# Kernel optimization log

Hardware: AMD Instinct MI355X
Metric: run time of the kernel (lower is better)

The kernel has to match this reference:

```python
import jax, jax.numpy as jnp
import numpy as np

B, S, D, H = 4, 1024, 1024, 16
DK = D // H


def _linear_params(key, scale):
    kw, kb = jax.random.split(key)
    W = jax.random.normal(kw, (D, D), dtype=jnp.float32) * scale
    b = jax.random.normal(kb, (D,), dtype=jnp.float32) * 0.01
    return W, b


def setup_inputs() -> dict:
    key = jax.random.key(0)
    ks = jax.random.split(key, 12)
    scale = 1.0 / np.sqrt(D)
    inp = {
        "query": jax.random.normal(ks[0], (B, S, D), dtype=jnp.float32),
        "key": jax.random.normal(ks[1], (B, S, D), dtype=jnp.float32),
        "value": jax.random.normal(ks[2], (B, S, D), dtype=jnp.float32),
        "time_k": jax.random.normal(ks[3], (B, S, D), dtype=jnp.float32),
        "time_v": jax.random.normal(ks[4], (B, S, D), dtype=jnp.float32),
        "mask": jnp.zeros((B, 1, S, S), dtype=jnp.float32),
    }
    names = ["Wq", "bq", "Wk", "bk", "Wv", "bv", "Wtk", "btk", "Wtv", "btv", "Wm", "bm"]
    for i in range(6):
        W, b = _linear_params(ks[5 + i], scale)
        inp[names[2 * i]] = W
        inp[names[2 * i + 1]] = b
    return inp


def _split_heads(x):
    # [B,S,D] -> [B,H,S,DK]
    b, s, _ = x.shape
    return x.reshape(b, s, H, DK).transpose(0, 2, 1, 3)


def reference(query, key, value, time_k, time_v, mask,
              Wq, bq, Wk, bk, Wv, bv, Wtk, btk, Wtv, btv, Wm, bm):
    q = _split_heads(query @ Wq + bq)
    k = _split_heads(key @ Wk + bk)
    v = _split_heads(value @ Wv + bv)
    t_k = _split_heads(time_k @ Wtk + btk)
    t_v = _split_heads(time_v @ Wtv + btv)

    # scores[b,h,i,j] = q_i . k_j + t_k_i . q_j  (note second term uses q on the key axis)
    scores = jnp.einsum("bhid,bhjd->bhij", q, k) + jnp.einsum("bhid,bhjd->bhij", t_k, q)
    # module divides by sqrt(d_model) (query.size(-1)), not sqrt(d_k)
    scores = scores / jnp.sqrt(jnp.float32(D)) + mask
    probs = jax.nn.softmax(scores, axis=-1)

    # dropout is identity (p=0 / eval); squeeze(-2) is a no-op for S>1
    context = jnp.einsum("bhij,bhjd->bhid", probs, v) + jnp.einsum("bhij,bhjd->bhid", probs, t_v)
    x = context.transpose(0, 2, 1, 3).reshape(query.shape[0], -1, D)
    return x @ Wm + bm
```

## Files before the change

kernel.cpp:

```cpp
#include <hip/hip_runtime.h>
#include <hip/hip_bf16.h>
#include <cstdint>
#include <cstddef>

typedef __bf16 bf16;
typedef bf16 bf16x8 __attribute__((ext_vector_type(8)));
typedef bf16 bf16x4 __attribute__((ext_vector_type(4)));
typedef float f32x4 __attribute__((ext_vector_type(4)));
typedef unsigned int u32;

#define DEV static __device__ __forceinline__

DEV f32x4 mfma16(bf16x8 a, bf16x8 b, f32x4 c) {
    return __builtin_amdgcn_mfma_f32_16x16x32_bf16(a, b, c, 0, 0, 0);
}

DEV f32x4 shflx4(f32x4 v, int m) {
    f32x4 r;
    for (int i = 0; i < 4; ++i) r[i] = __shfl_xor(v[i], m, 64);
    return r;
}

DEV bf16x8 cvt8(const float* p) {
    float4 f0 = *(const float4*)p;
    float4 f1 = *(const float4*)(p + 4);
    bf16x8 v;
    v[0] = (bf16)f0.x; v[1] = (bf16)f0.y; v[2] = (bf16)f0.z; v[3] = (bf16)f0.w;
    v[4] = (bf16)f1.x; v[5] = (bf16)f1.y; v[6] = (bf16)f1.z; v[7] = (bf16)f1.w;
    return v;
}

DEV void glo(const bf16* g, bf16* l) {
    __builtin_amdgcn_global_load_lds(
        (const __attribute__((address_space(1))) u32*)g,
        (__attribute__((address_space(3))) u32*)l,
        16, 0, 0);
}

struct PrepArgs {
    const float* w[6];
    const float* act[6];
    bf16* wt;
    bf16* actbf[6];
};

__global__ __launch_bounds__(256) void prep_kernel(PrepArgs p)
{
    const int z = blockIdx.z;
    const int t = threadIdx.x;
    if (z < 6) {
        __shared__ bf16 tile[64][72];
        const float* src = p.w[z];
        bf16* out = p.wt + (size_t)z * 1024 * 1024;
        const int r = t >> 3, c8 = (t & 7) * 8;
        const int row0 = blockIdx.y * 64, col0 = blockIdx.x * 64;
        *(bf16x8*)&tile[r][c8]      = cvt8(&src[(size_t)(row0 + r) * 1024 + col0 + c8]);
        *(bf16x8*)&tile[r + 32][c8] = cvt8(&src[(size_t)(row0 + r + 32) * 1024 + col0 + c8]);
        __syncthreads();
        for (int half = 0; half < 2; ++half) {
            int rr = r + half * 32;
            bf16x8 v;
            for (int j = 0; j < 8; ++j) v[j] = tile[c8 + j][rr];
            *(bf16x8*)&out[(size_t)(col0 + rr) * 1024 + row0 + c8] = v;
        }
    } else {
        const float* src = p.act[z - 6];
        bf16* dst = p.actbf[z - 6];
        const size_t chunk = (size_t)(blockIdx.y * 16 + blockIdx.x) * 16384;
        for (int c = 0; c < 8; ++c) {
            const size_t off = chunk + (size_t)c * 2048 + (size_t)t * 8;
            *(bf16x8*)&dst[off] = cvt8(&src[off]);
        }
    }
}

__global__ __launch_bounds__(256) void vsum_kernel(bf16* __restrict__ a,
                                                   const bf16* __restrict__ b)
{
    const size_t off = ((size_t)blockIdx.x * 256 + threadIdx.x) * 16;
    for (int c = 0; c < 2; ++c) {
        bf16x8 x = *(const bf16x8*)&a[off + c * 8];
        bf16x8 y = *(const bf16x8*)&b[off + c * 8];
        bf16x8 s;
        for (int e = 0; e < 8; ++e) s[e] = (bf16)((float)x[e] + (float)y[e]);
        *(bf16x8*)&a[off + c * 8] = s;
    }
}

struct ProjArgs {
    const void* A[5];
    const void* A2[5];
    const bf16* W[5];
    const bf16* W2[5];
    const float* bias[5];
    const float* bias2[5];
    bf16* out[5];
    int vst[5];
};

template<bool AF32>
__global__ __launch_bounds__(256) void proj_gemm(ProjArgs pa)
{
    const int z = blockIdx.z;
    const void* A   = pa.A[z];
    const void* A2p = pa.A2[z];
    const bf16* W   = pa.W[z];
    const bf16* W2  = pa.W2[z];
    const int m0 = blockIdx.y * 128, n0 = blockIdx.x * 128;
    __shared__ bf16 As[128 * 64];
    __shared__ bf16 Bs[128 * 64];
    const int t = threadIdx.x, lane = t & 63, w = t >> 6;
    const int ln = lane & 15, qd = lane >> 4;
    const int wm0 = (w >> 1) * 64, wn0 = (w & 1) * 64;
    const int srow = t >> 1, shalf = (t & 1) * 32;
    const int sub0 = w * 4;
    const int r8 = lane >> 3, c8 = (lane & 7) * 8;
    f32x4 acc[4][4];
    for (int i = 0; i < 4; ++i)
        for (int j = 0; j < 4; ++j)
            acc[i][j] = (f32x4){0.f, 0.f, 0.f, 0.f};
    const int npair = A2p ? 2 : 1;
    for (int pair = 0; pair < npair; ++pair) {
        const void* Ap = pair ? A2p : A;
        const bf16* Wp = pair ? W2 : W;
        for (int ks = 0; ks < 16; ++ks) {
            const int bk = ks * 64;
            __syncthreads();
            for (int i = 0; i < 4; ++i) {
                const int row = (sub0 + i) * 8 + r8;
                glo(&Wp[(size_t)(n0 + row) * 1024 + bk + c8], &Bs[(sub0 + i) * 512]);
            }
            if (AF32) {
                const float* src = &((const float*)Ap)[(size_t)(m0 + srow) * 1024 + bk + shalf];
                bf16* dst = &As[srow * 64 + shalf];
                *(bf16x8*)(dst)      = cvt8(src);
                *(bf16x8*)(dst + 8)  = cvt8(src + 8);
                *(bf16x8*)(dst + 16) = cvt8(src + 16);
                *(bf16x8*)(dst + 24) = cvt8(src + 24);
            } else {
                const bf16* Ab = (const bf16*)Ap;
                for (int i = 0; i < 4; ++i) {
                    const int row = (sub0 + i) * 8 + r8;
                    glo(&Ab[(size_t)(m0 + row) * 1024 + bk + c8], &As[(sub0 + i) * 512]);
                }
            }
            __syncthreads();
            for (int kc = 0; kc < 2; ++kc) {
                bf16x8 af[4], bfr[4];
                for (int mi = 0; mi < 4; ++mi)
                    af[mi] = *(const bf16x8*)&As[(wm0 + mi * 16 + ln) * 64 + kc * 32 + qd * 8];
                for (int ni = 0; ni < 4; ++ni)
                    bfr[ni] = *(const bf16x8*)&Bs[(wn0 + ni * 16 + ln) * 64 + kc * 32 + qd * 8];
                for (int mi = 0; mi < 4; ++mi)
                    for (int ni = 0; ni < 4; ++ni)
                        acc[mi][ni] = mfma16(af[mi], bfr[ni], acc[mi][ni]);
            }
        }
    }
    const float* bias  = pa.bias[z];
    const float* bias2 = pa.bias2[z];
    bf16* out = pa.out[z];
    const int vst = pa.vst[z];
    for (int ni = 0; ni < 4; ++ni) {
        const int n = n0 + wn0 + ni * 16 + ln;
        const float bv = bias[n] + (bias2 ? bias2[n] : 0.0f);
        for (int mi = 0; mi < 4; ++mi) {
            const int mbase = m0 + wm0 + mi * 16 + qd * 4;
            f32x4 v = acc[mi][ni];
            if (vst) {
                const int b = mbase >> 10, s = mbase & 1023;
                bf16x4 pk;
                for (int r = 0; r < 4; ++r) pk[r] = (bf16)(v[r] + bv);
                *(bf16x4*)&out[((size_t)(b * 1024 + n)) * 1024 + s] = pk;
            } else {
                for (int r = 0; r < 4; ++r)
                    out[(size_t)(mbase + r) * 1024 + n] = (bf16)(v[r] + bv);
            }
        }
    }
}

__global__ __launch_bounds__(256) void attn4_kernel(
    const bf16* __restrict__ Qb, const bf16* __restrict__ Kb, const bf16* __restrict__ TKb,
    const bf16* __restrict__ VsT, const bf16* __restrict__ maskbf,
    bf16* __restrict__ ctx)
{
    const int h = blockIdx.x, it = blockIdx.y, b = blockIdx.z;
    const int i0 = it * 128;
    __shared__ bf16 Ks[64 * 64];
    __shared__ bf16 QJs[64 * 64];
    __shared__ bf16 Vs[64 * 64];
    __shared__ bf16 Ms[128 * 64];
    __shared__ bf16 Ps[128][72];
    const int t = threadIdx.x, lane = t & 63, w = t >> 6;
    const int ln = lane & 15, qd = lane >> 4;
    const size_t baseQ = ((size_t)b * 1024) * 1024 + (size_t)h * 64;
    const size_t MMc = (size_t)1024 * 1024;

    bf16x8 qf[2][2], tkf[2][2];
    for (int si = 0; si < 2; ++si) {
        const size_t row = (size_t)(i0 + w * 32 + si * 16 + ln);
        for (int kc = 0; kc < 2; ++kc) {
            qf[si][kc]  = *(const bf16x8*)&Qb [baseQ + row * 1024 + kc * 32 + qd * 8];
            tkf[si][kc] = *(const bf16x8*)&TKb[baseQ + row * 1024 + kc * 32 + qd * 8];
        }
    }

    f32x4 O[2][4];
    f32x4 psum[2];
    for (int si = 0; si < 2; ++si) {
        psum[si] = (f32x4){0.f, 0.f, 0.f, 0.f};
        for (int dc = 0; dc < 4; ++dc) O[si][dc] = (f32x4){0.f, 0.f, 0.f, 0.f};
    }

    const float c1 = 0.045084439f;
    const float c2 = 1.442695041f;

    for (int jt = 0; jt < 16; ++jt) {
        const int j0 = jt * 64;
        __syncthreads();
        {
            const int rr = lane >> 3, cb = (lane & 7) * 8;
            for (int i = 0; i < 10; ++i) {
                const int u = w * 10 + i;
                if (u < 8) {
                    glo(&Kb[baseQ + (size_t)(j0 + u * 8 + rr) * 1024 + cb], &Ks[u * 512]);
                } else if (u < 16) {
                    const int s = u - 8;
                    glo(&Qb[baseQ + (size_t)(j0 + s * 8 + rr) * 1024 + cb], &QJs[s * 512]);
                } else if (u < 24) {
                    const int s = u - 16;
                    glo(&VsT[((size_t)b * 1024 + h * 64 + s * 8 + rr) * 1024 + j0 + cb],
                        &Vs[s * 512]);
                } else {
                    const int s = u - 24;
                    glo(&maskbf[(size_t)b * MMc + (size_t)(i0 + s * 8 + rr) * 1024 + j0 + cb],
                        &Ms[s * 512]);
                }
            }
        }
        __syncthreads();

        f32x4 sc[2][4];
        for (int jc = 0; jc < 4; ++jc) {
            bf16x8 kf[2], qjf[2];
            for (int kc = 0; kc < 2; ++kc) {
                kf[kc]  = *(const bf16x8*)&Ks [(jc * 16 + ln) * 64 + kc * 32 + qd * 8];
                qjf[kc] = *(const bf16x8*)&QJs[(jc * 16 + ln) * 64 + kc * 32 + qd * 8];
            }
            for (int si = 0; si < 2; ++si) {
                f32x4 a = (f32x4){0.f, 0.f, 0.f, 0.f};
                a = mfma16(qf[si][0], kf[0], a);
                a = mfma16(qf[si][1], kf[1], a);
                a = mfma16(tkf[si][0], qjf[0], a);
                a = mfma16(tkf[si][1], qjf[1], a);
                sc[si][jc] = a;
            }
        }
        for (int si = 0; si < 2; ++si) {
            const int ibl = w * 32 + si * 16 + qd * 4;
            for (int jc = 0; jc < 4; ++jc) {
                const int jl = jc * 16 + ln;
                for (int r = 0; r < 4; ++r) {
                    const float mv = (float)Ms[(ibl + r) * 64 + jl];
                    const float p = exp2f(fmaf(sc[si][jc][r], c1, mv * c2));
                    psum[si][r] += p;
                    Ps[ibl + r][jl] = (bf16)p;
                }
            }
        }
        for (int kc = 0; kc < 2; ++kc) {
            bf16x8 pa[2], vb[4];
            for (int si = 0; si < 2; ++si)
                pa[si] = *(const bf16x8*)&Ps[w * 32 + si * 16 + ln][kc * 32 + qd * 8];
            for (int dc = 0; dc < 4; ++dc)
                vb[dc] = *(const bf16x8*)&Vs[(dc * 16 + ln) * 64 + kc * 32 + qd * 8];
            for (int si = 0; si < 2; ++si)
                for (int dc = 0; dc < 4; ++dc)
                    O[si][dc] = mfma16(pa[si], vb[dc], O[si][dc]);
        }
    }

    for (int si = 0; si < 2; ++si) {
        for (int m = 1; m <= 8; m <<= 1) psum[si] += shflx4(psum[si], m);
        f32x4 rl;
        for (int r = 0; r < 4; ++r) rl[r] = 1.0f / psum[si][r];
        const int ibase = i0 + w * 32 + si * 16 + qd * 4;
        for (int dc = 0; dc < 4; ++dc) {
            const int d = h * 64 + dc * 16 + ln;
            f32x4 v = O[si][dc] * rl;
            for (int r = 0; r < 4; ++r)
                ctx[((size_t)b * 1024 + ibase + r) * 1024 + d] = (bf16)v[r];
        }
    }
}

__global__ __launch_bounds__(256) void out_gemm(
    const bf16* __restrict__ A, const bf16* __restrict__ W,
    const float* __restrict__ bias, float* __restrict__ out)
{
    const int n0 = blockIdx.x * 128, m0 = blockIdx.y * 64;
    __shared__ bf16 As[64 * 64];
    __shared__ bf16 Bs[128 * 64];
    const int t = threadIdx.x, lane = t & 63, w = t >> 6;
    const int ln = lane & 15, qd = lane >> 4;
    const int wn0 = w * 32;
    const int rr = lane >> 3, cb = (lane & 7) * 8;
    f32x4 acc[4][2];
    for (int i = 0; i < 4; ++i)
        for (int j = 0; j < 2; ++j)
            acc[i][j] = (f32x4){0.f, 0.f, 0.f, 0.f};
    for (int ks = 0; ks < 16; ++ks) {
        const int bk = ks * 64;
        __syncthreads();
        for (int i = 0; i < 6; ++i) {
            const int u = w * 6 + i;
            if (u < 8) {
                const int r8 = u * 8 + rr;
                glo(&A[(size_t)(m0 + r8) * 1024 + bk + cb], &As[u * 512]);
            } else {
                const int sub = u - 8, r8 = sub * 8 + rr;
                glo(&W[(size_t)(n0 + r8) * 1024 + bk + cb], &Bs[sub * 512]);
            }
        }
        __syncthreads();
        for (int kc = 0; kc < 2; ++kc) {
            bf16x8 af[4], bfr[2];
            for (int mi = 0; mi < 4; ++mi)
                af[mi] = *(const bf16x8*)&As[(mi * 16 + ln) * 64 + kc * 32 + qd * 8];
            for (int ni = 0; ni < 2; ++ni)
                bfr[ni] = *(const bf16x8*)&Bs[(wn0 + ni * 16 + ln) * 64 + kc * 32 + qd * 8];
            for (int mi = 0; mi < 4; ++mi)
                for (int ni = 0; ni < 2; ++ni)
                    acc[mi][ni] = mfma16(af[mi], bfr[ni], acc[mi][ni]);
        }
    }
    for (int ni = 0; ni < 2; ++ni) {
        const int n = n0 + wn0 + ni * 16 + ln;
        const float bv = bias[n];
        for (int mi = 0; mi < 4; ++mi) {
            const int mbase = m0 + mi * 16 + qd * 4;
            f32x4 v = acc[mi][ni];
            for (int r = 0; r < 4; ++r)
                out[(size_t)(mbase + r) * 1024 + n] = v[r] + bv;
        }
    }
}

extern "C" void kernel_launch(void* const* d_in, const int* in_sizes, int n_in,
                              void* d_out, int out_size, void* d_ws, size_t ws_size,
                              hipStream_t stream)
{
    (void)in_sizes; (void)n_in; (void)out_size;
    const float* query  = (const float*)d_in[0];
    const float* key    = (const float*)d_in[1];
    const float* value  = (const float*)d_in[2];
    const float* time_k = (const float*)d_in[3];
    const float* time_v = (const float*)d_in[4];
    const float* mask   = (const float*)d_in[5];
    const float* Wq  = (const float*)d_in[6];  const float* bq  = (const float*)d_in[7];
    const float* Wk  = (const float*)d_in[8];  const float* bk  = (const float*)d_in[9];
    const float* Wv  = (const float*)d_in[10]; const float* bv  = (const float*)d_in[11];
    const float* Wtk = (const float*)d_in[12]; const float* btk = (const float*)d_in[13];
    const float* Wtv = (const float*)d_in[14]; const float* btv = (const float*)d_in[15];
    const float* Wm  = (const float*)d_in[16]; const float* bm  = (const float*)d_in[17];

    bf16* ws = (bf16*)d_ws;
    const size_t MM = (size_t)1024 * 1024;
    bf16* WT = ws;
    bf16* maskbf = (bf16*)d_out;

    PrepArgs pp;
    pp.w[0] = Wq; pp.w[1] = Wk; pp.w[2] = Wv; pp.w[3] = Wtk; pp.w[4] = Wtv; pp.w[5] = Wm;
    pp.wt = WT;

    const bool big = ws_size >= (size_t)(46 * MM * sizeof(bf16));

    if (big) {
        bf16* qbf  = ws + 6 * MM;
        bf16* kbf  = ws + 10 * MM;
        bf16* vbf  = ws + 14 * MM;
        bf16* tkbf = ws + 18 * MM;
        bf16* tvbf = ws + 22 * MM;
        bf16* Qb   = ws + 26 * MM;
        bf16* Kb   = ws + 30 * MM;
        bf16* TKb  = ws + 34 * MM;
        bf16* VsTa = ws + 38 * MM;
        bf16* VsTb = ws + 42 * MM;
        bf16* ctx  = ws + 6 * MM;
        pp.act[0] = query; pp.act[1] = key; pp.act[2] = value;
        pp.act[3] = time_k; pp.act[4] = time_v; pp.act[5] = mask;
        pp.actbf[0] = qbf; pp.actbf[1] = kbf; pp.actbf[2] = vbf;
        pp.actbf[3] = tkbf; pp.actbf[4] = tvbf; pp.actbf[5] = maskbf;
        prep_kernel<<<dim3(16, 16, 12), 256, 0, stream>>>(pp);

        ProjArgs pa;
        for (int i = 0; i < 5; ++i) { pa.A2[i] = nullptr; pa.W2[i] = nullptr; pa.bias2[i] = nullptr; }
        pa.A[0] = qbf;  pa.W[0] = WT + 0 * MM; pa.bias[0] = bq;  pa.out[0] = Qb;   pa.vst[0] = 0;
        pa.A[1] = kbf;  pa.W[1] = WT + 1 * MM; pa.bias[1] = bk;  pa.out[1] = Kb;   pa.vst[1] = 0;
        pa.A[2] = tkbf; pa.W[2] = WT + 3 * MM; pa.bias[2] = btk; pa.out[2] = TKb;  pa.vst[2] = 0;
        pa.A[3] = vbf;  pa.W[3] = WT + 2 * MM; pa.bias[3] = bv;  pa.out[3] = VsTa; pa.vst[3] = 1;
        pa.A[4] = tvbf; pa.W[4] = WT + 4 * MM; pa.bias[4] = btv; pa.out[4] = VsTb; pa.vst[4] = 1;
        proj_gemm<false><<<dim3(8, 32, 5), 256, 0, stream>>>(pa);

        vsum_kernel<<<dim3(1024), 256, 0, stream>>>(VsTa, VsTb);
        attn4_kernel<<<dim3(16, 8, 4), 256, 0, stream>>>(
            Qb, Kb, TKb, VsTa, maskbf, ctx);
        out_gemm<<<dim3(8, 64), 256, 0, stream>>>(ctx, WT + 5 * MM, bm, (float*)d_out);
    } else {
        bf16* Qb  = ws + 6 * MM;
        bf16* Kb  = ws + 10 * MM;
        bf16* TKb = ws + 14 * MM;
        bf16* VsT = ws + 18 * MM;
        bf16* ctx = ws + 22 * MM;
        pp.act[0] = mask;
        for (int i = 1; i < 6; ++i) pp.act[i] = nullptr;
        pp.actbf[0] = maskbf;
        for (int i = 1; i < 6; ++i) pp.actbf[i] = nullptr;
        prep_kernel<<<dim3(16, 16, 7), 256, 0, stream>>>(pp);

        ProjArgs pa;
        for (int i = 0; i < 5; ++i) { pa.A2[i] = nullptr; pa.W2[i] = nullptr; pa.bias2[i] = nullptr; }
        pa.A[0] = value;  pa.A2[0] = time_v; pa.W[0] = WT + 2 * MM; pa.W2[0] = WT + 4 * MM;
        pa.bias[0] = bv;  pa.bias2[0] = btv; pa.out[0] = VsT; pa.vst[0] = 1;
        pa.A[1] = query;  pa.W[1] = WT + 0 * MM; pa.bias[1] = bq;  pa.out[1] = Qb;  pa.vst[1] = 0;
        pa.A[2] = key;    pa.W[2] = WT + 1 * MM; pa.bias[2] = bk;  pa.out[2] = Kb;  pa.vst[2] = 0;
        pa.A[3] = time_k; pa.W[3] = WT + 3 * MM; pa.bias[3] = btk; pa.out[3] = TKb; pa.vst[3] = 0;
        proj_gemm<true><<<dim3(8, 32, 4), 256, 0, stream>>>(pa);

        attn4_kernel<<<dim3(16, 8, 4), 256, 0, stream>>>(
            Qb, Kb, TKb, VsT, maskbf, ctx);
        out_gemm<<<dim3(8, 64), 256, 0, stream>>>(ctx, WT + 5 * MM, bm, (float*)d_out);
    }
}
```

Baseline: 344.3 us.

## Swizzle LDS tiles, pre-permute mask, fuse V sum into attention

Applies an XOR swizzle to the 16-byte chunks of every global_load_lds tile in the projection GEMM, attention and output GEMM to reduce LDS bank conflicts on MFMA operand reads. The mask is pre-permuted into each thread's register fragment layout by a new kernel, so attention loads it straight into registers instead of staging it in LDS. The separate vsum kernel is removed and V+TV is summed while filling the attention V tile, with padded rows for V and P. The small-workspace fallback path is removed and the big-workspace layout is always assumed.

```diff
diff --git a/kernel.cpp b/kernel.cpp
--- a/kernel.cpp
+++ b/kernel.cpp
@@ -37,11 +37,12 @@
         16, 0, 0);
 }
 
+
 struct PrepArgs {
     const float* w[6];
-    const float* act[6];
+    const float* act[5];
     bf16* wt;
-    bf16* actbf[6];
+    bf16* actbf[5];
 };
 
 __global__ __launch_bounds__(256) void prep_kernel(PrepArgs p)
@@ -74,96 +75,89 @@
     }
 }
 
-__global__ __launch_bounds__(256) void vsum_kernel(bf16* __restrict__ a,
-                                                   const bf16* __restrict__ b)
-{
-    const size_t off = ((size_t)blockIdx.x * 256 + threadIdx.x) * 16;
-    for (int c = 0; c < 2; ++c) {
-        bf16x8 x = *(const bf16x8*)&a[off + c * 8];
-        bf16x8 y = *(const bf16x8*)&b[off + c * 8];
-        bf16x8 s;
-        for (int e = 0; e < 8; ++e) s[e] = (bf16)((float)x[e] + (float)y[e]);
-        *(bf16x8*)&a[off + c * 8] = s;
-    }
+__global__ __launch_bounds__(256) void maskprep_kernel(
+    const float* __restrict__ mask, bf16* __restrict__ maskR)
+{
+    const int jt = blockIdx.x, it = blockIdx.y, b = blockIdx.z;
+    __shared__ bf16 Mt[128 * 72];
+    const int t = threadIdx.x, lane = t & 63, w = t >> 6;
+    const int ln = lane & 15, qd = lane >> 4;
+    {
+        const int il = t >> 1, jh = (t & 1) * 32;
+        const float* src = &mask[((size_t)b * 1024 + it * 128 + il) * 1024 + jt * 64 + jh];
+        *(bf16x8*)&Mt[il * 72 + jh]      = cvt8(src);
+        *(bf16x8*)&Mt[il * 72 + jh + 8]  = cvt8(src + 8);
+        *(bf16x8*)&Mt[il * 72 + jh + 16] = cvt8(src + 16);
+        *(bf16x8*)&Mt[il * 72 + jh + 24] = cvt8(src + 24);
+    }
+    __syncthreads();
+    bf16 m[32];
+    for (int si = 0; si < 2; ++si)
+        for (int jc = 0; jc < 4; ++jc)
+            for (int r = 0; r < 4; ++r) {
+                const int il = w * 32 + si * 16 + qd * 4 + r;
+                const int jl = jc * 16 + ln;
+                m[(si * 4 + jc) * 4 + r] = Mt[il * 72 + jl];
+            }
+    bf16* dst = &maskR[((((size_t)b * 8 + it) * 16 + jt) * 256 + t) * 32];
+    for (int c = 0; c < 4; ++c)
+        *(bf16x8*)&dst[c * 8] = *(const bf16x8*)&m[c * 8];
 }
 
 struct ProjArgs {
-    const void* A[5];
-    const void* A2[5];
+    const bf16* A[5];
     const bf16* W[5];
-    const bf16* W2[5];
     const float* bias[5];
-    const float* bias2[5];
     bf16* out[5];
     int vst[5];
 };
 
-template<bool AF32>
 __global__ __launch_bounds__(256) void proj_gemm(ProjArgs pa)
 {
     const int z = blockIdx.z;
-    const void* A   = pa.A[z];
-    const void* A2p = pa.A2[z];
-    const bf16* W   = pa.W[z];
-    const bf16* W2  = pa.W2[z];
+    const bf16* A = pa.A[z];
+    const bf16* W = pa.W[z];
     const int m0 = blockIdx.y * 128, n0 = blockIdx.x * 128;
     __shared__ bf16 As[128 * 64];
     __shared__ bf16 Bs[128 * 64];
     const int t = threadIdx.x, lane = t & 63, w = t >> 6;
     const int ln = lane & 15, qd = lane >> 4;
     const int wm0 = (w >> 1) * 64, wn0 = (w & 1) * 64;
-    const int srow = t >> 1, shalf = (t & 1) * 32;
     const int sub0 = w * 4;
-    const int r8 = lane >> 3, c8 = (lane & 7) * 8;
+    const int rr = lane >> 3;
+    const int cbs = (((lane & 7) ^ rr)) * 8;
+    const int lx = ln & 7;
     f32x4 acc[4][4];
     for (int i = 0; i < 4; ++i)
         for (int j = 0; j < 4; ++j)
             acc[i][j] = (f32x4){0.f, 0.f, 0.f, 0.f};
-    const int npair = A2p ? 2 : 1;
-    for (int pair = 0; pair < npair; ++pair) {
-        const void* Ap = pair ? A2p : A;
-        const bf16* Wp = pair ? W2 : W;
-        for (int ks = 0; ks < 16; ++ks) {
-            const int bk = ks * 64;
-            __syncthreads();
-            for (int i = 0; i < 4; ++i) {
-                const int row = (sub0 + i) * 8 + r8;
-                glo(&Wp[(size_t)(n0 + row) * 1024 + bk + c8], &Bs[(sub0 + i) * 512]);
-            }
-            if (AF32) {
-                const float* src = &((const float*)Ap)[(size_t)(m0 + srow) * 1024 + bk + shalf];
-                bf16* dst = &As[srow * 64 + shalf];
-                *(bf16x8*)(dst)      = cvt8(src);
-                *(bf16x8*)(dst + 8)  = cvt8(src + 8);
-                *(bf16x8*)(dst + 16) = cvt8(src + 16);
-                *(bf16x8*)(dst + 24) = cvt8(src + 24);
-            } else {
-                const bf16* Ab = (const bf16*)Ap;
-                for (int i = 0; i < 4; ++i) {
-                    const int row = (sub0 + i) * 8 + r8;
-                    glo(&Ab[(size_t)(m0 + row) * 1024 + bk + c8], &As[(sub0 + i) * 512]);
-                }
-            }
-            __syncthreads();
-            for (int kc = 0; kc < 2; ++kc) {
-                bf16x8 af[4], bfr[4];
-                for (int mi = 0; mi < 4; ++mi)
-                    af[mi] = *(const bf16x8*)&As[(wm0 + mi * 16 + ln) * 64 + kc * 32 + qd * 8];
+    for (int ks = 0; ks < 16; ++ks) {
+        const int bk = ks * 64;
+        __syncthreads();
+        for (int i = 0; i < 4; ++i) {
+            const int row = (sub0 + i) * 8 + rr;
+            glo(&W[(size_t)(n0 + row) * 1024 + bk + cbs], &Bs[(sub0 + i) * 512]);
+            glo(&A[(size_t)(m0 + row) * 1024 + bk + cbs], &As[(sub0 + i) * 512]);
+        }
+        __syncthreads();
+        for (int kc = 0; kc < 2; ++kc) {
+            const int sg = ((kc * 4 + qd) ^ lx) * 8;
+            bf16x8 af[4], bfr[4];
+            for (int mi = 0; mi < 4; ++mi)
+                af[mi] = *(const bf16x8*)&As[(wm0 + mi * 16 + ln) * 64 + sg];
+            for (int ni = 0; ni < 4; ++ni)
+                bfr[ni] = *(const bf16x8*)&Bs[(wn0 + ni * 16 + ln) * 64 + sg];
+            for (int mi = 0; mi < 4; ++mi)
                 for (int ni = 0; ni < 4; ++ni)
-                    bfr[ni] = *(const bf16x8*)&Bs[(wn0 + ni * 16 + ln) * 64 + kc * 32 + qd * 8];
-                for (int mi = 0; mi < 4; ++mi)
-                    for (int ni = 0; ni < 4; ++ni)
-                        acc[mi][ni] = mfma16(af[mi], bfr[ni], acc[mi][ni]);
-            }
-        }
-    }
-    const float* bias  = pa.bias[z];
-    const float* bias2 = pa.bias2[z];
+                    acc[mi][ni] = mfma16(af[mi], bfr[ni], acc[mi][ni]);
+        }
+    }
+    const float* bias = pa.bias[z];
     bf16* out = pa.out[z];
     const int vst = pa.vst[z];
     for (int ni = 0; ni < 4; ++ni) {
         const int n = n0 + wn0 + ni * 16 + ln;
-        const float bv = bias[n] + (bias2 ? bias2[n] : 0.0f);
+        const float bv = bias[n];
         for (int mi = 0; mi < 4; ++mi) {
             const int mbase = m0 + wm0 + mi * 16 + qd * 4;
             f32x4 v = acc[mi][ni];
@@ -180,22 +174,21 @@
     }
 }
 
-__global__ __launch_bounds__(256) void attn4_kernel(
+__global__ __launch_bounds__(256) void attn6_kernel(
     const bf16* __restrict__ Qb, const bf16* __restrict__ Kb, const bf16* __restrict__ TKb,
-    const bf16* __restrict__ VsT, const bf16* __restrict__ maskbf,
-    bf16* __restrict__ ctx)
+    const bf16* __restrict__ Va, const bf16* __restrict__ Vb,
+    const bf16* __restrict__ maskR, bf16* __restrict__ ctx)
 {
     const int h = blockIdx.x, it = blockIdx.y, b = blockIdx.z;
     const int i0 = it * 128;
     __shared__ bf16 Ks[64 * 64];
     __shared__ bf16 QJs[64 * 64];
-    __shared__ bf16 Vs[64 * 64];
-    __shared__ bf16 Ms[128 * 64];
-    __shared__ bf16 Ps[128][72];
+    __shared__ bf16 Vs[64 * 68];
+    __shared__ bf16 Ps[128][68];
     const int t = threadIdx.x, lane = t & 63, w = t >> 6;
     const int ln = lane & 15, qd = lane >> 4;
+    const int lx = ln & 7;
     const size_t baseQ = ((size_t)b * 1024) * 1024 + (size_t)h * 64;
-    const size_t MMc = (size_t)1024 * 1024;
 
     bf16x8 qf[2][2], tkf[2][2];
     for (int si = 0; si < 2; ++si) {
@@ -216,28 +209,44 @@
     const float c1 = 0.045084439f;
     const float c2 = 1.442695041f;
 
+    const size_t mtile0 = (((size_t)b * 8 + it) * 16) * 256 + t;
+
     for (int jt = 0; jt < 16; ++jt) {
         const int j0 = jt * 64;
         __syncthreads();
         {
-            const int rr = lane >> 3, cb = (lane & 7) * 8;
-            for (int i = 0; i < 10; ++i) {
-                const int u = w * 10 + i;
+            const int rr = lane >> 3;
+            const int cbs = ((lane & 7) ^ rr) * 8;
+            for (int i = 0; i < 4; ++i) {
+                const int u = w * 4 + i;
                 if (u < 8) {
-                    glo(&Kb[baseQ + (size_t)(j0 + u * 8 + rr) * 1024 + cb], &Ks[u * 512]);
-                } else if (u < 16) {
+                    glo(&Kb[baseQ + (size_t)(j0 + u * 8 + rr) * 1024 + cbs], &Ks[u * 512]);
+                } else {
                     const int s = u - 8;
-                    glo(&Qb[baseQ + (size_t)(j0 + s * 8 + rr) * 1024 + cb], &QJs[s * 512]);
-                } else if (u < 24) {
-                    const int s = u - 16;
-                    glo(&VsT[((size_t)b * 1024 + h * 64 + s * 8 + rr) * 1024 + j0 + cb],
-                        &Vs[s * 512]);
-                } else {
-                    const int s = u - 24;
-                    glo(&maskbf[(size_t)b * MMc + (size_t)(i0 + s * 8 + rr) * 1024 + j0 + cb],
-                        &Ms[s * 512]);
+                    glo(&Qb[baseQ + (size_t)(j0 + s * 8 + rr) * 1024 + cbs], &QJs[s * 512]);
                 }
             }
+        }
+        {
+            const int vrow = t >> 2, vcol = (t & 3) * 16;
+            const size_t va = ((size_t)b * 1024 + h * 64 + vrow) * 1024 + j0 + vcol;
+            bf16x8 a0 = *(const bf16x8*)&Va[va];
+            bf16x8 a1 = *(const bf16x8*)&Va[va + 8];
+            bf16x8 b0 = *(const bf16x8*)&Vb[va];
+            bf16x8 b1 = *(const bf16x8*)&Vb[va + 8];
+            bf16 s[16];
+            for (int e = 0; e < 8; ++e) {
+                s[e]     = (bf16)((float)a0[e] + (float)b0[e]);
+                s[8 + e] = (bf16)((float)a1[e] + (float)b1[e]);
+            }
+            bf16* dst = &Vs[vrow * 68 + vcol];
+            for (int c = 0; c < 4; ++c)
+                *(bf16x4*)&dst[c * 4] = *(const bf16x4*)&s[c * 4];
+        }
+        bf16x8 mm[4];
+        {
+            const bf16* mb = &maskR[(mtile0 + (size_t)jt * 256) * 32];
+            for (int c = 0; c < 4; ++c) mm[c] = *(const bf16x8*)&mb[c * 8];
         }
         __syncthreads();
 
@@ -245,8 +254,9 @@
         for (int jc = 0; jc < 4; ++jc) {
             bf16x8 kf[2], qjf[2];
             for (int kc = 0; kc < 2; ++kc) {
-                kf[kc]  = *(const bf16x8*)&Ks [(jc * 16 + ln) * 64 + kc * 32 + qd * 8];
-                qjf[kc] = *(const bf16x8*)&QJs[(jc * 16 + ln) * 64 + kc * 32 + qd * 8];
+                const int sg = ((kc * 4 + qd) ^ lx) * 8;
+                kf[kc]  = *(const bf16x8*)&Ks [(jc * 16 + ln) * 64 + sg];
+                qjf[kc] = *(const bf16x8*)&QJs[(jc * 16 + ln) * 64 + sg];
             }
             for (int si = 0; si < 2; ++si) {
                 f32x4 a = (f32x4){0.f, 0.f, 0.f, 0.f};
@@ -261,9 +271,10 @@
             const int ibl = w * 32 + si * 16 + qd * 4;
             for (int jc = 0; jc < 4; ++jc) {
                 const int jl = jc * 16 + ln;
+                const int e = si * 4 + jc;
                 for (int r = 0; r < 4; ++r) {
-                    const float mv = (float)Ms[(ibl + r) * 64 + jl];
-                    const float p = exp2f(fmaf(sc[si][jc][r], c1, mv * c2));
+                    const float mval = (float)mm[e >> 1][(e & 1) * 4 + r];
+                    const float p = exp2f(fmaf(sc[si][jc][r], c1, mval * c2));
                     psum[si][r] += p;
                     Ps[ibl + r][jl] = (bf16)p;
                 }
@@ -271,10 +282,16 @@
         }
         for (int kc = 0; kc < 2; ++kc) {
             bf16x8 pa[2], vb[4];
-            for (int si = 0; si < 2; ++si)
-                pa[si] = *(const bf16x8*)&Ps[w * 32 + si * 16 + ln][kc * 32 + qd * 8];
-            for (int dc = 0; dc < 4; ++dc)
-                vb[dc] = *(const bf16x8*)&Vs[(dc * 16 + ln) * 64 + kc * 32 + qd * 8];
+            for (int si = 0; si < 2; ++si) {
+                bf16x4 lo = *(const bf16x4*)&Ps[w * 32 + si * 16 + ln][kc * 32 + qd * 8];
+                bf16x4 hi = *(const bf16x4*)&Ps[w * 32 + si * 16 + ln][kc * 32 + qd * 8 + 4];
+                for (int e = 0; e < 4; ++e) { pa[si][e] = lo[e]; pa[si][4 + e] = hi[e]; }
+            }
+            for (int dc = 0; dc < 4; ++dc) {
+                bf16x4 lo = *(const bf16x4*)&Vs[(dc * 16 + ln) * 68 + kc * 32 + qd * 8];
+                bf16x4 hi = *(const bf16x4*)&Vs[(dc * 16 + ln) * 68 + kc * 32 + qd * 8 + 4];
+                for (int e = 0; e < 4; ++e) { vb[dc][e] = lo[e]; vb[dc][4 + e] = hi[e]; }
+            }
             for (int si = 0; si < 2; ++si)
                 for (int dc = 0; dc < 4; ++dc)
                     O[si][dc] = mfma16(pa[si], vb[dc], O[si][dc]);
@@ -305,7 +322,9 @@
     const int t = threadIdx.x, lane = t & 63, w = t >> 6;
     const int ln = lane & 15, qd = lane >> 4;
     const int wn0 = w * 32;
-    const int rr = lane >> 3, cb = (lane & 7) * 8;
+    const int rr = lane >> 3;
+    const int cbs = ((lane & 7) ^ rr) * 8;
+    const int lx = ln & 7;
     f32x4 acc[4][2];
     for (int i = 0; i < 4; ++i)
         for (int j = 0; j < 2; ++j)
@@ -316,20 +335,20 @@
         for (int i = 0; i < 6; ++i) {
             const int u = w * 6 + i;
             if (u < 8) {
-                const int r8 = u * 8 + rr;
-                glo(&A[(size_t)(m0 + r8) * 1024 + bk + cb], &As[u * 512]);
+                glo(&A[(size_t)(m0 + u * 8 + rr) * 1024 + bk + cbs], &As[u * 512]);
             } else {
-                const int sub = u - 8, r8 = sub * 8 + rr;
-                glo(&W[(size_t)(n0 + r8) * 1024 + bk + cb], &Bs[sub * 512]);
+                const int sub = u - 8;
+                glo(&W[(size_t)(n0 + sub * 8 + rr) * 1024 + bk + cbs], &Bs[sub * 512]);
             }
         }
         __syncthreads();
         for (int kc = 0; kc < 2; ++kc) {
+            const int sg = ((kc * 4 + qd) ^ lx) * 8;
             bf16x8 af[4], bfr[2];
             for (int mi = 0; mi < 4; ++mi)
-                af[mi] = *(const bf16x8*)&As[(mi * 16 + ln) * 64 + kc * 32 + qd * 8];
+                af[mi] = *(const bf16x8*)&As[(mi * 16 + ln) * 64 + sg];
             for (int ni = 0; ni < 2; ++ni)
-                bfr[ni] = *(const bf16x8*)&Bs[(wn0 + ni * 16 + ln) * 64 + kc * 32 + qd * 8];
+                bfr[ni] = *(const bf16x8*)&Bs[(wn0 + ni * 16 + ln) * 64 + sg];
             for (int mi = 0; mi < 4; ++mi)
                 for (int ni = 0; ni < 2; ++ni)
                     acc[mi][ni] = mfma16(af[mi], bfr[ni], acc[mi][ni]);
@@ -351,7 +370,7 @@
                               void* d_out, int out_size, void* d_ws, size_t ws_size,
                               hipStream_t stream)
 {
-    (void)in_sizes; (void)n_in; (void)out_size;
+    (void)in_sizes; (void)n_in; (void)out_size; (void)ws_size;
     const float* query  = (const float*)d_in[0];
     const float* key    = (const float*)d_in[1];
     const float* value  = (const float*)d_in[2];
@@ -367,69 +386,39 @@
 
     bf16* ws = (bf16*)d_ws;
     const size_t MM = (size_t)1024 * 1024;
-    bf16* WT = ws;
-    bf16* maskbf = (bf16*)d_out;
+    bf16* WT    = ws;
+    bf16* qbf   = ws + 6 * MM;
+    bf16* kbf   = ws + 10 * MM;
+    bf16* vbf   = ws + 14 * MM;
+    bf16* tkbf  = ws + 18 * MM;
+    bf16* tvbf  = ws + 22 * MM;
+    bf16* Qb    = ws + 26 * MM;
+    bf16* Kb    = ws + 30 * MM;
+    bf16* TKb   = ws + 34 * MM;
+    bf16* VsTa  = ws + 38 * MM;
+    bf16* VsTb  = ws + 42 * MM;
+    bf16* ctx   = ws + 6 * MM;
+    bf16* maskR = (bf16*)d_out;
 
     PrepArgs pp;
     pp.w[0] = Wq; pp.w[1] = Wk; pp.w[2] = Wv; pp.w[3] = Wtk; pp.w[4] = Wtv; pp.w[5] = Wm;
     pp.wt = WT;
-
-    const bool big = ws_size >= (size_t)(46 * MM * sizeof(bf16));
-
-    if (big) {
-        bf16* qbf  = ws + 6 * MM;
-        bf16* kbf  = ws + 10 * MM;
-        bf16* vbf  = ws + 14 * MM;
-        bf16* tkbf = ws + 18 * MM;
-        bf16* tvbf = ws + 22 * MM;
-        bf16* Qb   = ws + 26 * MM;
-        bf16* Kb   = ws + 30 * MM;
-        bf16* TKb  = ws + 34 * MM;
-        bf16* VsTa = ws + 38 * MM;
-        bf16* VsTb = ws + 42 * MM;
-        bf16* ctx  = ws + 6 * MM;
-        pp.act[0] = query; pp.act[1] = key; pp.act[2] = value;
-        pp.act[3] = time_k; pp.act[4] = time_v; pp.act[5] = mask;
-        pp.actbf[0] = qbf; pp.actbf[1] = kbf; pp.actbf[2] = vbf;
-        pp.actbf[3] = tkbf; pp.actbf[4] = tvbf; pp.actbf[5] = maskbf;
-        prep_kernel<<<dim3(16, 16, 12), 256, 0, stream>>>(pp);
-
-        ProjArgs pa;
-        for (int i = 0; i < 5; ++i) { pa.A2[i] = nullptr; pa.W2[i] = nullptr; pa.bias2[i] = nullptr; }
-        pa.A[0] = qbf;  pa.W[0] = WT + 0 * MM; pa.bias[0] = bq;  pa.out[0] = Qb;   pa.vst[0] = 0;
-        pa.A[1] = kbf;  pa.W[1] = WT + 1 * MM; pa.bias[1] = bk;  pa.out[1] = Kb;   pa.vst[1] = 0;
-        pa.A[2] = tkbf; pa.W[2] = WT + 3 * MM; pa.bias[2] = btk; pa.out[2] = TKb;  pa.vst[2] = 0;
-        pa.A[3] = vbf;  pa.W[3] = WT + 2 * MM; pa.bias[3] = bv;  pa.out[3] = VsTa; pa.vst[3] = 1;
-        pa.A[4] = tvbf; pa.W[4] = WT + 4 * MM; pa.bias[4] = btv; pa.out[4] = VsTb; pa.vst[4] = 1;
-        proj_gemm<false><<<dim3(8, 32, 5), 256, 0, stream>>>(pa);
-
-        vsum_kernel<<<dim3(1024), 256, 0, stream>>>(VsTa, VsTb);
-        attn4_kernel<<<dim3(16, 8, 4), 256, 0, stream>>>(
-            Qb, Kb, TKb, VsTa, maskbf, ctx);
-        out_gemm<<<dim3(8, 64), 256, 0, stream>>>(ctx, WT + 5 * MM, bm, (float*)d_out);
-    } else {
-        bf16* Qb  = ws + 6 * MM;
-        bf16* Kb  = ws + 10 * MM;
-        bf16* TKb = ws + 14 * MM;
-        bf16* VsT = ws + 18 * MM;
-        bf16* ctx = ws + 22 * MM;
-        pp.act[0] = mask;
-        for (int i = 1; i < 6; ++i) pp.act[i] = nullptr;
-        pp.actbf[0] = maskbf;
-        for (int i = 1; i < 6; ++i) pp.actbf[i] = nullptr;
-        prep_kernel<<<dim3(16, 16, 7), 256, 0, stream>>>(pp);
-
-        ProjArgs pa;
-        for (int i = 0; i < 5; ++i) { pa.A2[i] = nullptr; pa.W2[i] = nullptr; pa.bias2[i] = nullptr; }
-        pa.A[0] = value;  pa.A2[0] = time_v; pa.W[0] = WT + 2 * MM; pa.W2[0] = WT + 4 * MM;
-        pa.bias[0] = bv;  pa.bias2[0] = btv; pa.out[0] = VsT; pa.vst[0] = 1;
-        pa.A[1] = query;  pa.W[1] = WT + 0 * MM; pa.bias[1] = bq;  pa.out[1] = Qb;  pa.vst[1] = 0;
-        pa.A[2] = key;    pa.W[2] = WT + 1 * MM; pa.bias[2] = bk;  pa.out[2] = Kb;  pa.vst[2] = 0;
-        pa.A[3] = time_k; pa.W[3] = WT + 3 * MM; pa.bias[3] = btk; pa.out[3] = TKb; pa.vst[3] = 0;
-        proj_gemm<true><<<dim3(8, 32, 4), 256, 0, stream>>>(pa);
-
-        attn4_kernel<<<dim3(16, 8, 4), 256, 0, stream>>>(
-            Qb, Kb, TKb, VsT, maskbf, ctx);
-        out_gemm<<<dim3(8, 64), 256, 0, stream>>>(ctx, WT + 5 * MM, bm, (float*)d_out);
-    }
-}
+    pp.act[0] = query; pp.act[1] = key; pp.act[2] = value;
+    pp.act[3] = time_k; pp.act[4] = time_v;
+    pp.actbf[0] = qbf; pp.actbf[1] = kbf; pp.actbf[2] = vbf;
+    pp.actbf[3] = tkbf; pp.actbf[4] = tvbf;
+    prep_kernel<<<dim3(16, 16, 11), 256, 0, stream>>>(pp);
+    maskprep_kernel<<<dim3(16, 8, 4), 256, 0, stream>>>(mask, maskR);
+
+    ProjArgs pa;
+    pa.A[0] = qbf;  pa.W[0] = WT + 0 * MM; pa.bias[0] = bq;  pa.out[0] = Qb;   pa.vst[0] = 0;
+    pa.A[1] = kbf;  pa.W[1] = WT + 1 * MM; pa.bias[1] = bk;  pa.out[1] = Kb;   pa.vst[1] = 0;
+    pa.A[2] = tkbf; pa.W[2] = WT + 3 * MM; pa.bias[2] = btk; pa.out[2] = TKb;  pa.vst[2] = 0;
+    pa.A[3] = vbf;  pa.W[3] = WT + 2 * MM; pa.bias[3] = bv;  pa.out[3] = VsTa; pa.vst[3] = 1;
+    pa.A[4] = tvbf; pa.W[4] = WT + 4 * MM; pa.bias[4] = btv; pa.out[4] = VsTb; pa.vst[4] = 1;
+    proj_gemm<<<dim3(8, 32, 5), 256, 0, stream>>>(pa);
+
+    attn6_kernel<<<dim3(16, 8, 4), 256, 0, stream>>>(
+        Qb, Kb, TKb, VsTa, VsTb, maskR, ctx);
+    out_gemm<<<dim3(8, 64), 256, 0, stream>>>(ctx, WT + 5 * MM, bm, (float*)d_out);
+}
```

Result: faster. 326.9 us (-5.1%).
